# Optimization experiments

Measured on AMD Instinct MI355X. Metric: run time of the kernel, lower is better.

## Reference

```python
import jax, jax.numpy as jnp
import numpy as np

V = 100000; E = 512; HD = 512; S = 2048; T = 12; START = 10; STOP = 11
NEG = -10000.0


def setup_inputs() -> dict:
    key = jax.random.key(0)
    ks = jax.random.split(key, 16)
    n = lambda k, sh, s=0.1: jax.random.normal(k, sh, dtype=jnp.float32) * s
    trans = jax.random.normal(ks[14], (T, T), dtype=jnp.float32)
    trans = trans.at[START, :].set(NEG).at[:, STOP].set(NEG)
    return {
        "sentence": jax.random.randint(ks[0], (S,), 0, V),
        "embed": jax.random.normal(ks[1], (V, E), dtype=jnp.float32),
        "Wih_f": n(ks[2], (4 * HD, E)), "Whh_f": n(ks[3], (4 * HD, HD)),
        "bih_f": n(ks[4], (4 * HD,)), "bhh_f": n(ks[5], (4 * HD,)),
        "Wih_b": n(ks[6], (4 * HD, E)), "Whh_b": n(ks[7], (4 * HD, HD)),
        "bih_b": n(ks[8], (4 * HD,)), "bhh_b": n(ks[9], (4 * HD,)),
        "h0": jax.random.normal(ks[10], (2, 1, HD), dtype=jnp.float32),
        "c0": jax.random.normal(ks[11], (2, 1, HD), dtype=jnp.float32),
        "W_out": n(ks[12], (T, 2 * HD)), "b_out": n(ks[13], (T,)),
        "transitions": trans,
    }


def _lstm_dir(x, Wih, Whh, bih, bhh, h0, c0):
    # PyTorch LSTM cell: gates ordered (i, f, g, o)
    def step(carry, xt):
        h, c = carry
        g = xt @ Wih.T + bih + h @ Whh.T + bhh
        i, f, gg, o = jnp.split(g, 4)
        c = jax.nn.sigmoid(f) * c + jax.nn.sigmoid(i) * jnp.tanh(gg)
        h = jax.nn.sigmoid(o) * jnp.tanh(c)
        return (h, c), h
    _, hs = jax.lax.scan(step, (h0, c0), x)
    return hs  # [S, HD]


def reference(sentence, embed, Wih_f, Whh_f, bih_f, bhh_f,
              Wih_b, Whh_b, bih_b, bhh_b, h0, c0, W_out, b_out, transitions):
    emb = embed[sentence]                                        # [S, E]
    hf = _lstm_dir(emb, Wih_f, Whh_f, bih_f, bhh_f, h0[0, 0], c0[0, 0])
    hb = _lstm_dir(emb[::-1], Wih_b, Whh_b, bih_b, bhh_b, h0[1, 0], c0[1, 0])[::-1]
    feats = jnp.concatenate([hf, hb], axis=-1) @ W_out.T + b_out  # [S, T]

    # Viterbi decode, vectorized over the tag dimension
    fv0 = jnp.full((T,), NEG, dtype=feats.dtype).at[START].set(0.0)

    def vstep(fv, feat):
        scores = fv[None, :] + transitions     # [next_tag, prev_tag]
        bp = jnp.argmax(scores, axis=1)
        return jnp.max(scores, axis=1) + feat, bp

    fv, bptrs = jax.lax.scan(vstep, fv0, feats)  # bptrs: [S, T]
    terminal = fv + transitions[STOP]
    best = jnp.argmax(terminal)
    path_score = terminal[best]

    def btrace(tag, bp):
        return bp[tag], tag

    _, best_path = jax.lax.scan(btrace, best, bptrs, reverse=True)  # [S]
    return path_score, best_path
```

## Files before the change

### kernel.cpp

```cpp
#include <hip/hip_runtime.h>
#include <math.h>

#define S_LEN 2048
#define HD 512
#define E_DIM 512
#define NTAG 12
#define TAG_START 10
#define TAG_STOP 11
#define NEGV -10000.0f

#define SENT 0x7F7F7F7Fu

__global__ __attribute__((amdgpu_flat_work_group_size(256, 256), amdgpu_waves_per_eu(1, 1)))
void lstm_rec(
    const float* __restrict__ WhhF, const float* __restrict__ WhhB,
    const float* __restrict__ WihF, const float* __restrict__ WihB,
    const float* __restrict__ bihF, const float* __restrict__ bhhF,
    const float* __restrict__ bihB, const float* __restrict__ bhhB,
    const int* __restrict__ sent, const float* __restrict__ embed,
    const float* __restrict__ h0, const float* __restrict__ c0,
    unsigned* __restrict__ hfp, unsigned* __restrict__ hbp)
{
    const int bid = blockIdx.x;
    const int dir = bid >> 6;
    const int b   = bid & 63;
    const float* __restrict__ Whh = dir ? WhhB : WhhF;
    const float* __restrict__ Wih = dir ? WihB : WihF;
    const float* __restrict__ bih = dir ? bihB : bihF;
    const float* __restrict__ bhh = dir ? bhhB : bhhF;
    unsigned* __restrict__ Hu = dir ? hbp : hfp;

    const int tid = threadIdx.x;
    const int r = tid >> 3;
    const int k = tid & 7;
    const int ul = r >> 2;
    const int g = r & 3;
    const int unit = b * 8 + ul;
    const int row_g = g * HD + unit;

    const float4* wp = (const float4*)(Whh + (size_t)row_g * HD + k * 64);
    const float4* up = (const float4*)(Wih + (size_t)row_g * E_DIM + k * 64);
#define WDECL(i) float4 w##i = wp[i]; float4 u##i = up[i];
    WDECL(0)  WDECL(1)  WDECL(2)  WDECL(3)
    WDECL(4)  WDECL(5)  WDECL(6)  WDECL(7)
    WDECL(8)  WDECL(9)  WDECL(10) WDECL(11)
    WDECL(12) WDECL(13) WDECL(14) WDECL(15)
#define WPIN(i) asm volatile("" : "+v"(w##i.x), "+v"(w##i.y), "+v"(w##i.z), "+v"(w##i.w), \
                                  "+v"(u##i.x), "+v"(u##i.y), "+v"(u##i.z), "+v"(u##i.w));
    WPIN(0)  WPIN(1)  WPIN(2)  WPIN(3)
    WPIN(4)  WPIN(5)  WPIN(6)  WPIN(7)
    WPIN(8)  WPIN(9)  WPIN(10) WPIN(11)
    WPIN(12) WPIN(13) WPIN(14) WPIN(15)

    __shared__ float hlds[2][8 * 68];
    __shared__ float elds[2][8 * 68];

    const int l  = tid & 63;
    const int l0 = l & 32;
    const bool cellln = (l & 31) == 0;
    float c = cellln ? c0[dir*HD + unit] : 0.f;

    float xval = 0.f;
    if (k == 0) xval = bih[row_g] + bhh[row_g];

    const int ch  = tid >> 5;
    const int off = (tid * 2) & 63;

    float2 ereg;
    {
        const int t0 = dir ? (S_LEN-1) : 0;
        const float2 ev = ((const float2*)(embed + (size_t)sent[t0] * E_DIM))[tid];
        elds[0][ch*68 + off]   = ev.x;
        elds[0][ch*68 + off+1] = ev.y;
        const int t1 = dir ? (S_LEN-2) : 1;
        ereg = ((const float2*)(embed + (size_t)sent[t1] * E_DIM))[tid];
    }

    for (int s = 0; s < S_LEN; ++s) {
        const int t_io = dir ? (S_LEN-1-s) : s;
        float* __restrict__ hl = hlds[s & 1];

        {
            float* __restrict__ el = elds[(s+1) & 1];
            el[ch*68 + off]   = ereg.x;
            el[ch*68 + off+1] = ereg.y;
        }

        if (s == 0) {
            float2 hv = *(const float2*)(h0 + dir*HD + tid*2);
            hl[ch*68 + off]   = hv.x;
            hl[ch*68 + off+1] = hv.y;
        } else {
            const int prev = dir ? (t_io+1) : (t_io-1);
            const unsigned long long* src =
                (const unsigned long long*)(Hu + (size_t)prev*HD) + tid;
            unsigned long long v;
            do {
                v = __hip_atomic_load(src, __ATOMIC_RELAXED, __HIP_MEMORY_SCOPE_AGENT);
            } while ((unsigned)v == SENT || (unsigned)(v >> 32) == SENT);
            hl[ch*68 + off]   = __uint_as_float((unsigned)v);
            hl[ch*68 + off+1] = __uint_as_float((unsigned)(v >> 32));
        }
        __syncthreads();

        if (s + 2 < S_LEN) {
            const int t2 = dir ? (t_io - 2) : (t_io + 2);
            ereg = ((const float2*)(embed + (size_t)sent[t2] * E_DIM))[tid];
        }

        float a0 = 0.f, a1 = 0.f, a2 = 0.f, a3 = 0.f;
        const float* __restrict__ hp = &hl[k * 68];
        const float* __restrict__ ep = &elds[s & 1][k * 68];
#define WDOT(i) { const float4 hv = *(const float4*)(hp + 4*(i)); \
        a0 += w##i.x*hv.x; a1 += w##i.y*hv.y; a2 += w##i.z*hv.z; a3 += w##i.w*hv.w; } \
        { const float4 ev4 = *(const float4*)(ep + 4*(i)); \
        a0 += u##i.x*ev4.x; a1 += u##i.y*ev4.y; a2 += u##i.z*ev4.z; a3 += u##i.w*ev4.w; }
        WDOT(0)  WDOT(1)  WDOT(2)  WDOT(3)
        WDOT(4)  WDOT(5)  WDOT(6)  WDOT(7)
        WDOT(8)  WDOT(9)  WDOT(10) WDOT(11)
        WDOT(12) WDOT(13) WDOT(14) WDOT(15)
        float acc = (a0 + a1) + (a2 + a3);

        acc += __shfl_xor(acc, 1);
        acc += __shfl_xor(acc, 2);
        acc += __shfl_xor(acc, 4);
        const float pre = acc + xval;

        const float yy  = (g == 2) ? 2.f*pre : pre;
        const float sg  = 1.f / (1.f + __expf(-yy));
        const float act = (g == 2) ? 2.f*sg - 1.f : sg;

        const float a_i = __shfl(act, l0 + 0);
        const float a_f = __shfl(act, l0 + 8);
        const float a_g = __shfl(act, l0 + 16);
        const float a_o = __shfl(act, l0 + 24);

        float hval = 0.f;
        if (cellln) {
            c = a_f*c + a_i*a_g;
            const float th = 2.f / (1.f + __expf(-2.f*c)) - 1.f;
            hval = a_o * th;
        }
        const float h_hi = __shfl(hval, l0 ? 96 : 32, 64);
        if (l == 0) {
            const unsigned long long pv =
                (unsigned long long)__float_as_uint(hval) |
                ((unsigned long long)__float_as_uint(h_hi) << 32);
            unsigned long long* dst =
                (unsigned long long*)(Hu + (size_t)t_io*HD) + (unit >> 1);
            __hip_atomic_store(dst, pv, __ATOMIC_RELAXED, __HIP_MEMORY_SCOPE_AGENT);
        }
        __syncthreads();
    }
}

__global__ __launch_bounds__(256) void feats_k(
    const float* __restrict__ hf, const float* __restrict__ hb,
    const float* __restrict__ Wout, const float* __restrict__ bout,
    float* __restrict__ feats)
{
    int idx = blockIdx.x * blockDim.x + threadIdx.x;
    if (idx >= S_LEN * NTAG) return;
    int t = idx / NTAG, tag = idx - t*NTAG;
    const float* __restrict__ wf  = Wout + (size_t)tag * (2*HD);
    const float* __restrict__ ha  = hf + (size_t)t * HD;
    const float* __restrict__ hbr = hb + (size_t)t * HD;
    float a0=0.f, a1=0.f, a2=0.f, a3=0.f;
    for (int i = 0; i < HD; i += 4) {
        float4 h4 = *(const float4*)(ha + i);
        float4 w4 = *(const float4*)(wf + i);
        a0 += h4.x*w4.x; a1 += h4.y*w4.y; a2 += h4.z*w4.z; a3 += h4.w*w4.w;
    }
    for (int i = 0; i < HD; i += 4) {
        float4 h4 = *(const float4*)(hbr + i);
        float4 w4 = *(const float4*)(wf + HD + i);
        a0 += h4.x*w4.x; a1 += h4.y*w4.y; a2 += h4.z*w4.z; a3 += h4.w*w4.w;
    }
    feats[idx] = a0+a1+a2+a3 + bout[tag];
}

__global__ __launch_bounds__(256, 1) void viterbi_k(
    const float* __restrict__ feats, const float* __restrict__ trans,
    float* __restrict__ out)
{
    __shared__ float fl[S_LEN * NTAG];
    __shared__ unsigned char bpl[S_LEN * NTAG];
    {
        const float4* src = (const float4*)feats;
        float4* dst = (float4*)fl;
        for (int i = threadIdx.x; i < S_LEN*NTAG/4; i += 256) dst[i] = src[i];
    }
    __syncthreads();
    if (threadIdx.x < 64) {
        const int ln = threadIdx.x;
        if (ln < NTAG) {
            float tr[NTAG];
            #pragma unroll
            for (int p = 0; p < NTAG; ++p) tr[p] = trans[ln*NTAG + p];
            float fv = (ln == TAG_START) ? 0.f : NEGV;
            for (int t = 0; t < S_LEN; ++t) {
                float best = -3.4e38f; int arg = 0;
                #pragma unroll
                for (int p = 0; p < NTAG; ++p) {
                    float sc = __shfl(fv, p) + tr[p];
                    if (sc > best) { best = sc; arg = p; }
                }
                bpl[t*NTAG + ln] = (unsigned char)arg;
                fv = best + fl[t*NTAG + ln];
            }
            float tsc = fv + trans[TAG_STOP*NTAG + ln];
            float bestt = -3.4e38f; int argt = 0;
            #pragma unroll
            for (int p = 0; p < NTAG; ++p) {
                float v = __shfl(tsc, p);
                if (v > bestt) { bestt = v; argt = p; }
            }
            if (ln == 0) {
                out[0] = bestt;
                int tag = argt;
                for (int t = S_LEN-1; t >= 0; --t) {
                    out[1+t] = (float)tag;
                    tag = bpl[t*NTAG + tag];
                }
            }
        }
    }
}

extern "C" void kernel_launch(void* const* d_in, const int* in_sizes, int n_in,
                              void* d_out, int out_size, void* d_ws, size_t ws_size,
                              hipStream_t stream)
{
    const int*   sent  = (const int*)d_in[0];
    const float* embed = (const float*)d_in[1];
    const float* WihF  = (const float*)d_in[2];
    const float* WhhF  = (const float*)d_in[3];
    const float* bihF  = (const float*)d_in[4];
    const float* bhhF  = (const float*)d_in[5];
    const float* WihB  = (const float*)d_in[6];
    const float* WhhB  = (const float*)d_in[7];
    const float* bihB  = (const float*)d_in[8];
    const float* bhhB  = (const float*)d_in[9];
    const float* h0    = (const float*)d_in[10];
    const float* c0    = (const float*)d_in[11];
    const float* Wout  = (const float*)d_in[12];
    const float* bout  = (const float*)d_in[13];
    const float* trans = (const float*)d_in[14];
    float* out = (float*)d_out;

    float* ws = (float*)d_ws;
    float* hf = ws;
    float* hb = hf + (size_t)S_LEN * HD;
    float* feats = hb + (size_t)S_LEN * HD;

    hipMemsetAsync(hf, 0x7F, (size_t)2 * S_LEN * HD * sizeof(float), stream);
    lstm_rec<<<128, 256, 0, stream>>>(WhhF, WhhB, WihF, WihB,
                                      bihF, bhhF, bihB, bhhB,
                                      sent, embed, h0, c0,
                                      (unsigned*)hf, (unsigned*)hb);
    {
        int n = S_LEN * NTAG;
        feats_k<<<(n + 255)/256, 256, 0, stream>>>(hf, hb, Wout, bout, feats);
    }
    viterbi_k<<<1, 256, 0, stream>>>(feats, trans, out);
}
```

Baseline: 4.964 ms.

## Parallelize Viterbi via chunked max-plus scan and drop a per-step LSTM barrier

The serial 2048-step Viterbi forward pass is replaced by a chunked max-plus scan. Each of 256 chunks computes a 12x12 transfer matrix in parallel, one small kernel scans the chunks, then backpointers are rebuilt per chunk in parallel before a serial backtrace. In the LSTM recurrence, the embedding LDS store moves after the barrier and the trailing __syncthreads is removed, cutting one barrier per timestep. This adds three extra kernel launches and relies on double-buffered LDS being safe with only one barrier per step.

```diff
diff --git a/kernel.cpp b/kernel.cpp
--- a/kernel.cpp
+++ b/kernel.cpp
@@ -8,6 +8,9 @@
 #define TAG_START 10
 #define TAG_STOP 11
 #define NEGV -10000.0f
+
+#define NCHUNK 256
+#define CLEN 8
 
 #define SENT 0x7F7F7F7Fu
 
@@ -79,12 +82,6 @@
     for (int s = 0; s < S_LEN; ++s) {
         const int t_io = dir ? (S_LEN-1-s) : s;
         float* __restrict__ hl = hlds[s & 1];
-
-        {
-            float* __restrict__ el = elds[(s+1) & 1];
-            el[ch*68 + off]   = ereg.x;
-            el[ch*68 + off+1] = ereg.y;
-        }
 
         if (s == 0) {
             float2 hv = *(const float2*)(h0 + dir*HD + tid*2);
@@ -103,6 +100,11 @@
         }
         __syncthreads();
 
+        {
+            float* __restrict__ el = elds[(s+1) & 1];
+            el[ch*68 + off]   = ereg.x;
+            el[ch*68 + off+1] = ereg.y;
+        }
         if (s + 2 < S_LEN) {
             const int t2 = dir ? (t_io - 2) : (t_io + 2);
             ereg = ((const float2*)(embed + (size_t)sent[t2] * E_DIM))[tid];
@@ -150,7 +152,6 @@
                 (unsigned long long*)(Hu + (size_t)t_io*HD) + (unit >> 1);
             __hip_atomic_store(dst, pv, __ATOMIC_RELAXED, __HIP_MEMORY_SCOPE_AGENT);
         }
-        __syncthreads();
     }
 }
 
@@ -179,50 +180,115 @@
     feats[idx] = a0+a1+a2+a3 + bout[tag];
 }
 
-__global__ __launch_bounds__(256, 1) void viterbi_k(
+__global__ __launch_bounds__(64) void vit_chunk(
     const float* __restrict__ feats, const float* __restrict__ trans,
-    float* __restrict__ out)
-{
-    __shared__ float fl[S_LEN * NTAG];
-    __shared__ unsigned char bpl[S_LEN * NTAG];
+    float* __restrict__ Cws)
+{
+    const int chunk = blockIdx.x;
+    const int j = threadIdx.x;
+    __shared__ float tr[NTAG*NTAG];
+    for (int i = threadIdx.x; i < NTAG*NTAG; i += 64) tr[i] = trans[i];
+    __syncthreads();
+    if (j >= NTAG) return;
+
+    const int t0 = chunk * CLEN;
+    float c[NTAG];
     {
-        const float4* src = (const float4*)feats;
-        float4* dst = (float4*)fl;
-        for (int i = threadIdx.x; i < S_LEN*NTAG/4; i += 256) dst[i] = src[i];
+        const float* f0 = feats + (size_t)t0 * NTAG;
+        #pragma unroll
+        for (int i = 0; i < NTAG; ++i) c[i] = tr[i*NTAG + j] + f0[i];
+    }
+    for (int t = 1; t < CLEN; ++t) {
+        const float* ft = feats + (size_t)(t0 + t) * NTAG;
+        float cn[NTAG];
+        #pragma unroll
+        for (int i = 0; i < NTAG; ++i) {
+            float m = tr[i*NTAG + 0] + c[0];
+            #pragma unroll
+            for (int k = 1; k < NTAG; ++k) m = fmaxf(m, tr[i*NTAG + k] + c[k]);
+            cn[i] = m + ft[i];
+        }
+        #pragma unroll
+        for (int i = 0; i < NTAG; ++i) c[i] = cn[i];
+    }
+    #pragma unroll
+    for (int i = 0; i < NTAG; ++i) Cws[(size_t)chunk*NTAG*NTAG + i*NTAG + j] = c[i];
+}
+
+__global__ __launch_bounds__(64) void vit_scan(
+    const float* __restrict__ Cws, float* __restrict__ fvs)
+{
+    const int i = threadIdx.x;
+    float fv[NTAG];
+    #pragma unroll
+    for (int p = 0; p < NTAG; ++p) fv[p] = (p == TAG_START) ? 0.f : NEGV;
+
+    for (int c = 0; c < NCHUNK; ++c) {
+        if (i < NTAG) fvs[c*16 + i] = fv[i];
+        float m = -3.4e38f;
+        if (i < NTAG) {
+            const float* row = Cws + (size_t)c*NTAG*NTAG + i*NTAG;
+            #pragma unroll
+            for (int j = 0; j < NTAG; ++j) m = fmaxf(m, row[j] + fv[j]);
+        }
+        #pragma unroll
+        for (int p = 0; p < NTAG; ++p) fv[p] = __shfl(m, p);
+    }
+    if (i < NTAG) fvs[NCHUNK*16 + i] = fv[i];
+}
+
+__global__ __launch_bounds__(64) void vit_bp(
+    const float* __restrict__ feats, const float* __restrict__ trans,
+    const float* __restrict__ fvs, unsigned char* __restrict__ bp)
+{
+    const int chunk = blockIdx.x;
+    const int ln = threadIdx.x;
+    float tr[NTAG];
+    float fv = 0.f;
+    if (ln < NTAG) {
+        #pragma unroll
+        for (int p = 0; p < NTAG; ++p) tr[p] = trans[ln*NTAG + p];
+        fv = fvs[chunk*16 + ln];
+    }
+    const int t0 = chunk * CLEN;
+    for (int t = 0; t < CLEN; ++t) {
+        float sc[NTAG];
+        #pragma unroll
+        for (int p = 0; p < NTAG; ++p) sc[p] = __shfl(fv, p) + tr[p];
+        float best = sc[0]; int arg = 0;
+        #pragma unroll
+        for (int p = 1; p < NTAG; ++p)
+            if (sc[p] > best) { best = sc[p]; arg = p; }
+        if (ln < NTAG) {
+            bp[(size_t)(t0 + t)*16 + ln] = (unsigned char)arg;
+            fv = best + feats[(size_t)(t0 + t)*NTAG + ln];
+        }
+    }
+}
+
+__global__ __launch_bounds__(256) void vit_bt(
+    const unsigned char* __restrict__ bp, const float* __restrict__ fvs,
+    const float* __restrict__ trans, float* __restrict__ out)
+{
+    __shared__ unsigned char bpl[S_LEN * 16];
+    {
+        const float4* src = (const float4*)bp;
+        float4* dst = (float4*)bpl;
+        for (int i = threadIdx.x; i < S_LEN*16/16; i += 256) dst[i] = src[i];
     }
     __syncthreads();
-    if (threadIdx.x < 64) {
-        const int ln = threadIdx.x;
-        if (ln < NTAG) {
-            float tr[NTAG];
-            #pragma unroll
-            for (int p = 0; p < NTAG; ++p) tr[p] = trans[ln*NTAG + p];
-            float fv = (ln == TAG_START) ? 0.f : NEGV;
-            for (int t = 0; t < S_LEN; ++t) {
-                float best = -3.4e38f; int arg = 0;
-                #pragma unroll
-                for (int p = 0; p < NTAG; ++p) {
-                    float sc = __shfl(fv, p) + tr[p];
-                    if (sc > best) { best = sc; arg = p; }
-                }
-                bpl[t*NTAG + ln] = (unsigned char)arg;
-                fv = best + fl[t*NTAG + ln];
-            }
-            float tsc = fv + trans[TAG_STOP*NTAG + ln];
-            float bestt = -3.4e38f; int argt = 0;
-            #pragma unroll
-            for (int p = 0; p < NTAG; ++p) {
-                float v = __shfl(tsc, p);
-                if (v > bestt) { bestt = v; argt = p; }
-            }
-            if (ln == 0) {
-                out[0] = bestt;
-                int tag = argt;
-                for (int t = S_LEN-1; t >= 0; --t) {
-                    out[1+t] = (float)tag;
-                    tag = bpl[t*NTAG + tag];
-                }
-            }
+    if (threadIdx.x == 0) {
+        float best = -3.4e38f; int arg = 0;
+        #pragma unroll
+        for (int i = 0; i < NTAG; ++i) {
+            const float v = fvs[NCHUNK*16 + i] + trans[TAG_STOP*NTAG + i];
+            if (v > best) { best = v; arg = i; }
+        }
+        out[0] = best;
+        int tag = arg;
+        for (int t = S_LEN-1; t >= 0; --t) {
+            out[1+t] = (float)tag;
+            tag = bpl[t*16 + tag];
         }
     }
 }
@@ -249,9 +315,12 @@
     float* out = (float*)d_out;
 
     float* ws = (float*)d_ws;
-    float* hf = ws;
-    float* hb = hf + (size_t)S_LEN * HD;
+    float* hf    = ws;
+    float* hb    = hf + (size_t)S_LEN * HD;
     float* feats = hb + (size_t)S_LEN * HD;
+    float* Cws   = feats + (size_t)S_LEN * NTAG;
+    float* fvs   = Cws + (size_t)NCHUNK * NTAG * NTAG;
+    unsigned char* bp = (unsigned char*)(fvs + (size_t)(NCHUNK+1) * 16);
 
     hipMemsetAsync(hf, 0x7F, (size_t)2 * S_LEN * HD * sizeof(float), stream);
     lstm_rec<<<128, 256, 0, stream>>>(WhhF, WhhB, WihF, WihB,
@@ -262,5 +331,8 @@
         int n = S_LEN * NTAG;
         feats_k<<<(n + 255)/256, 256, 0, stream>>>(hf, hb, Wout, bout, feats);
     }
-    viterbi_k<<<1, 256, 0, stream>>>(feats, trans, out);
-}
+    vit_chunk<<<NCHUNK, 64, 0, stream>>>(feats, trans, Cws);
+    vit_scan<<<1, 64, 0, stream>>>(Cws, fvs);
+    vit_bp<<<NCHUNK, 64, 0, stream>>>(feats, trans, fvs, bp);
+    vit_bt<<<1, 256, 0, stream>>>(bp, fvs, trans, out);
+}
```

After: 6.406 ms. 29.0% more time.
